# Kernel tuning notes

Measured on AMD Instinct MI355X. Metric: run time of the kernel, lower is better.

The kernel has to match this reference:

```python
import jax, jax.numpy as jnp
import numpy as np

B, M, P, OUT_DIM, DIM = 4096, 128, 3, 256, 3  # batch, n_ctrl_pts, degree, eval points, coord dim
KNOTS = M + P + 1  # clamped knot vector length = 132


def setup_inputs() -> dict:
    key = jax.random.key(0)
    k1, k2 = jax.random.split(key)
    ctrl_pts = jax.random.normal(k1, (B, M, DIM), dtype=jnp.float32)
    # Clamped, nondecreasing knot vector in [0,1]: (p+1) zeros, sorted interior, (p+1) ones.
    interior = jnp.sort(jax.random.uniform(k2, (B, M - P - 1), dtype=jnp.float32), axis=1)
    knot_u = jnp.concatenate(
        [jnp.zeros((B, P + 1), jnp.float32), interior, jnp.ones((B, P + 1), jnp.float32)],
        axis=1,
    )
    return {"ctrl_pts": ctrl_pts, "knot_u": knot_u}


def reference(ctrl_pts, knot_u):
    p = P
    U = knot_u  # [B, m+p+1]
    u = jnp.linspace(1e-05, 1.0 - 1e-05, OUT_DIM, dtype=jnp.float32)  # [T] shared across batch

    # --- knot-span search (argmin of masked positive differences, first occurrence) ---
    d = u[None, None, :] - U[:, p:, None]            # [B, m+1, T]
    masked = jnp.where(d > 1e-08, d, 1.0)
    uspan = jnp.argmin(masked, axis=1) + p           # [B, T], int

    # --- Cox-de Boor basis recursion (degree 0 .. p) ---
    Ni = [None] * (p + 1)
    Ni[0] = jnp.ones((U.shape[0], OUT_DIM), jnp.float32)
    for k in range(1, p + 1):
        saved = jnp.zeros((U.shape[0], OUT_DIM), jnp.float32)
        for r in range(k):
            U1 = jnp.take_along_axis(U, uspan + r + 1, axis=1)      # U[s, uspan + r + 1]
            U2 = jnp.take_along_axis(U, uspan + 1 - k + r, axis=1)  # U[s, uspan + 1 - k + r]
            dU = (U1 - u) + (u - U2)
            dU_ = jnp.where(dU == 0.0, 1e-04, dU)
            temp = Ni[r] / dU_
            temp = jnp.where(dU == 0.0, 1e-04, temp)
            Ni[r] = saved + (U1 - u) * temp
            saved = (u - U2) * temp
        Ni[k] = saved
    Nu = jnp.stack(Ni, axis=-1)  # [B, T, p+1] nonzero basis values

    # --- sparse combine: instead of scattering into a [B,T,m] matrix and a dense matmul,
    # gather the (p+1) active control points per eval point (same math: all other
    # basis entries are zero) ---
    idx = uspan[:, :, None] + jnp.arange(-p, 1)                     # [B, T, p+1]
    cp = ctrl_pts[jnp.arange(U.shape[0])[:, None, None], idx]      # [B, T, p+1, DIM]
    return jnp.einsum('btk,btkd->btd', Nu, cp.astype(jnp.float32))  # [B, T, DIM]
```

## Files before the change

kernel.cpp:

```cpp
#include <hip/hip_runtime.h>


#define B_N     4096
#define M_N     128
#define P_DEG   3
#define T_N     256
#define KNOTS_N 132

__global__ __launch_bounds__(256) void curve_eval_kernel(
    const float* __restrict__ ctrl,
    const float* __restrict__ knots,
    float* __restrict__ out)
{
    __shared__ float Uk[KNOTS_N];
    __shared__ float cp[M_N * 3];

    const int b = blockIdx.x;
    const int t = threadIdx.x;

    if (t < KNOTS_N) Uk[t] = knots[(size_t)b * KNOTS_N + t];
    for (int i = t; i < M_N * 3; i += 256) cp[i] = ctrl[(size_t)b * M_N * 3 + i];
    __syncthreads();

    const double start = 1e-5;
    const double stop  = 1.0 - 1e-5;
    const double step  = (stop - start) / 255.0;
    float u;
    if (t == T_N - 1) u = (float)stop;
    else              u = (float)((double)t * step + start);

    int lo = 0, hi = 128;
    while (lo < hi) {
        int mid = (lo + hi + 1) >> 1;
        float d = __fsub_rn(u, Uk[P_DEG + mid]);
        if (d > 1e-8f) lo = mid; else hi = mid - 1;
    }
    const float dmin = __fsub_rn(u, Uk[P_DEG + lo]);
    while (lo > 0 && __fsub_rn(u, Uk[P_DEG + lo - 1]) == dmin) --lo;
    const int span = lo + P_DEG;

    float Ni[P_DEG + 1];
    Ni[0] = 1.0f;
    #pragma unroll
    for (int k = 1; k <= P_DEG; ++k) {
        float saved = 0.0f;
        #pragma unroll
        for (int r = 0; r < k; ++r) {
            const float U1 = Uk[span + r + 1];
            const float U2 = Uk[span + 1 - k + r];
            const float a1 = __fsub_rn(U1, u);
            const float a2 = __fsub_rn(u, U2);
            const float dU = __fadd_rn(a1, a2);
            const float dU_ = (dU == 0.0f) ? 1e-4f : dU;
            float temp = __fdiv_rn(Ni[r], dU_);
            if (dU == 0.0f) temp = 1e-4f;
            Ni[r] = __fadd_rn(saved, __fmul_rn(a1, temp));
            saved = __fmul_rn(a2, temp);
        }
        Ni[k] = saved;
    }

    float acc0 = 0.0f, acc1 = 0.0f, acc2 = 0.0f;
    #pragma unroll
    for (int k = 0; k <= P_DEG; ++k) {
        const int row = span - P_DEG + k;
        const float w = Ni[k];
        acc0 = __fadd_rn(acc0, __fmul_rn(w, cp[row * 3 + 0]));
        acc1 = __fadd_rn(acc1, __fmul_rn(w, cp[row * 3 + 1]));
        acc2 = __fadd_rn(acc2, __fmul_rn(w, cp[row * 3 + 2]));
    }

    float* o = out + ((size_t)b * T_N + t) * 3;
    o[0] = acc0;
    o[1] = acc1;
    o[2] = acc2;
}

extern "C" void kernel_launch(void* const* d_in, const int* in_sizes, int n_in,
                              void* d_out, int out_size, void* d_ws, size_t ws_size,
                              hipStream_t stream) {
    const float* ctrl  = (const float*)d_in[0];
    const float* knots = (const float*)d_in[1];
    float* out = (float*)d_out;

    curve_eval_kernel<<<dim3(B_N), dim3(T_N), 0, stream>>>(ctrl, knots, out);
}
```

Before: 13.63 us.

## Vectorize shared loads, pad control points to float4, use fast reciprocal in Cox-de Boor

Knots and control points are loaded into shared memory with float4 global reads, and control points are repacked into a 4-float stride so the gather of the four active points becomes four float4 LDS reads. The Cox-de Boor recursion is hand-unrolled with the knot differences hoisted once. The IEEE division is replaced by a multiply with the hardware reciprocal approximation. This cuts load instructions and division cost, but the approximate reciprocal can differ from the reference in the last bits.

```diff
diff --git a/kernel.cpp b/kernel.cpp
--- a/kernel.cpp
+++ b/kernel.cpp
@@ -13,13 +13,22 @@
     float* __restrict__ out)
 {
     __shared__ float Uk[KNOTS_N];
-    __shared__ float cp[M_N * 3];
+    __shared__ float cp[M_N * 4];
 
     const int b = blockIdx.x;
     const int t = threadIdx.x;
 
-    if (t < KNOTS_N) Uk[t] = knots[(size_t)b * KNOTS_N + t];
-    for (int i = t; i < M_N * 3; i += 256) cp[i] = ctrl[(size_t)b * M_N * 3 + i];
+    if (t < 33) {
+        ((float4*)Uk)[t] = ((const float4*)(knots + (size_t)b * KNOTS_N))[t];
+    }
+    if (t < 96) {
+        float4 v = ((const float4*)(ctrl + (size_t)b * (M_N * 3)))[t];
+        int i = t * 4;
+        cp[((i + 0) / 3) * 4 + (i + 0) % 3] = v.x;
+        cp[((i + 1) / 3) * 4 + (i + 1) % 3] = v.y;
+        cp[((i + 2) / 3) * 4 + (i + 2) % 3] = v.z;
+        cp[((i + 3) / 3) * 4 + (i + 3) % 3] = v.w;
+    }
     __syncthreads();
 
     const double start = 1e-5;
@@ -35,40 +44,75 @@
         float d = __fsub_rn(u, Uk[P_DEG + mid]);
         if (d > 1e-8f) lo = mid; else hi = mid - 1;
     }
-    const float dmin = __fsub_rn(u, Uk[P_DEG + lo]);
-    while (lo > 0 && __fsub_rn(u, Uk[P_DEG + lo - 1]) == dmin) --lo;
+    {
+        const float dmin = __fsub_rn(u, Uk[P_DEG + lo]);
+        while (lo > 0 && __fsub_rn(u, Uk[P_DEG + lo - 1]) == dmin) --lo;
+    }
     const int span = lo + P_DEG;
 
-    float Ni[P_DEG + 1];
-    Ni[0] = 1.0f;
-    #pragma unroll
-    for (int k = 1; k <= P_DEG; ++k) {
-        float saved = 0.0f;
-        #pragma unroll
-        for (int r = 0; r < k; ++r) {
-            const float U1 = Uk[span + r + 1];
-            const float U2 = Uk[span + 1 - k + r];
-            const float a1 = __fsub_rn(U1, u);
-            const float a2 = __fsub_rn(u, U2);
-            const float dU = __fadd_rn(a1, a2);
-            const float dU_ = (dU == 0.0f) ? 1e-4f : dU;
-            float temp = __fdiv_rn(Ni[r], dU_);
-            if (dU == 0.0f) temp = 1e-4f;
-            Ni[r] = __fadd_rn(saved, __fmul_rn(a1, temp));
-            saved = __fmul_rn(a2, temp);
+    const float w0 = Uk[span - 2];
+    const float w1 = Uk[span - 1];
+    const float w2 = Uk[span];
+    const float w3 = Uk[span + 1];
+    const float w4 = Uk[span + 2];
+    const float w5 = Uk[span + 3];
+
+    const float A1 = __fsub_rn(w3, u);
+    const float A2 = __fsub_rn(w4, u);
+    const float A3 = __fsub_rn(w5, u);
+    const float B0 = __fsub_rn(u, w0);
+    const float B1 = __fsub_rn(u, w1);
+    const float B2 = __fsub_rn(u, w2);
+
+    #define TDIV(N_, a1_, a2_, OUT_)                                    \
+        {                                                               \
+            const float dU = __fadd_rn(a1_, a2_);                       \
+            float tmp = __fmul_rn((N_), __builtin_amdgcn_rcpf(dU));     \
+            if (dU == 0.0f) tmp = 1e-4f;                                \
+            OUT_ = tmp;                                                 \
         }
-        Ni[k] = saved;
-    }
 
-    float acc0 = 0.0f, acc1 = 0.0f, acc2 = 0.0f;
-    #pragma unroll
-    for (int k = 0; k <= P_DEG; ++k) {
-        const int row = span - P_DEG + k;
-        const float w = Ni[k];
-        acc0 = __fadd_rn(acc0, __fmul_rn(w, cp[row * 3 + 0]));
-        acc1 = __fadd_rn(acc1, __fmul_rn(w, cp[row * 3 + 1]));
-        acc2 = __fadd_rn(acc2, __fmul_rn(w, cp[row * 3 + 2]));
-    }
+    float t0, t1, t2;
+    float N0, N1, N2, N3, saved;
+
+    TDIV(1.0f, A1, B2, t0);
+    N0 = __fmul_rn(A1, t0);
+    N1 = __fmul_rn(B2, t0);
+    TDIV(N0, A1, B1, t0);
+    TDIV(N1, A2, B2, t1);
+    N0    = __fmul_rn(A1, t0);
+    saved = __fmul_rn(B1, t0);
+    N1    = __fadd_rn(saved, __fmul_rn(A2, t1));
+    N2    = __fmul_rn(B2, t1);
+    TDIV(N0, A1, B0, t0);
+    TDIV(N1, A2, B1, t1);
+    TDIV(N2, A3, B2, t2);
+    N0    = __fmul_rn(A1, t0);
+    saved = __fmul_rn(B0, t0);
+    N1    = __fadd_rn(saved, __fmul_rn(A2, t1));
+    saved = __fmul_rn(B1, t1);
+    N2    = __fadd_rn(saved, __fmul_rn(A3, t2));
+    N3    = __fmul_rn(B2, t2);
+    #undef TDIV
+
+    const float4 c0 = *(const float4*)&cp[(span - 3) * 4];
+    const float4 c1 = *(const float4*)&cp[(span - 2) * 4];
+    const float4 c2 = *(const float4*)&cp[(span - 1) * 4];
+    const float4 c3 = *(const float4*)&cp[(span - 0) * 4];
+
+    float acc0, acc1, acc2;
+    acc0 = __fmul_rn(N0, c0.x);
+    acc1 = __fmul_rn(N0, c0.y);
+    acc2 = __fmul_rn(N0, c0.z);
+    acc0 = __fadd_rn(acc0, __fmul_rn(N1, c1.x));
+    acc1 = __fadd_rn(acc1, __fmul_rn(N1, c1.y));
+    acc2 = __fadd_rn(acc2, __fmul_rn(N1, c1.z));
+    acc0 = __fadd_rn(acc0, __fmul_rn(N2, c2.x));
+    acc1 = __fadd_rn(acc1, __fmul_rn(N2, c2.y));
+    acc2 = __fadd_rn(acc2, __fmul_rn(N2, c2.z));
+    acc0 = __fadd_rn(acc0, __fmul_rn(N3, c3.x));
+    acc1 = __fadd_rn(acc1, __fmul_rn(N3, c3.y));
+    acc2 = __fadd_rn(acc2, __fmul_rn(N3, c3.z));
 
     float* o = out + ((size_t)b * T_N + t) * 3;
     o[0] = acc0;
```

Result: faster. 11.93 us (median of 2 runs) (-12.5%).
